# Kernel tuning notes

Measured on AMD Instinct MI355X. Metric: run time of the kernel, lower is better.

Reference implementation:

```python
import jax, jax.numpy as jnp
import numpy as np

N_NODES = 50000
N_EDGES = 800000
IN_CH = 128
HIDDEN = 64
OUT_CH = 32
N_REL = 8
N_GRAPHS = 64
NEG_SLOPE = 0.2  # RGATConv default leaky_relu slope


def setup_inputs() -> dict:
    key = jax.random.key(0)
    ks = jax.random.split(key, 20)
    s = 0.05
    inp = {
        "x": jax.random.normal(ks[0], (N_NODES, IN_CH), dtype=jnp.float32),
        "edge_index": jax.random.randint(ks[1], (2, N_EDGES), 0, N_NODES, dtype=jnp.int64),
        "edge_type": jax.random.randint(ks[2], (N_EDGES,), 0, N_REL, dtype=jnp.int64),
        "batch": jnp.sort(jax.random.randint(ks[3], (N_NODES,), 0, N_GRAPHS, dtype=jnp.int64)),
        # encoder Linear(in, hidden)
        "enc_W": jax.random.normal(ks[4], (IN_CH, HIDDEN), dtype=jnp.float32) * s,
        "enc_b": jnp.zeros((HIDDEN,), dtype=jnp.float32),
        # RGAT layer 0 (hidden -> hidden), heads=1, dim=1
        "w0": jax.random.normal(ks[5], (N_REL, HIDDEN, HIDDEN), dtype=jnp.float32) * s,
        "q0": jax.random.normal(ks[6], (HIDDEN, 1), dtype=jnp.float32) * s,
        "k0": jax.random.normal(ks[7], (HIDDEN, 1), dtype=jnp.float32) * s,
        "b0": jnp.zeros((HIDDEN,), dtype=jnp.float32),
        # RGAT layer 1 (hidden -> hidden)
        "w1": jax.random.normal(ks[8], (N_REL, HIDDEN, HIDDEN), dtype=jnp.float32) * s,
        "q1": jax.random.normal(ks[9], (HIDDEN, 1), dtype=jnp.float32) * s,
        "k1": jax.random.normal(ks[10], (HIDDEN, 1), dtype=jnp.float32) * s,
        "b1": jnp.zeros((HIDDEN,), dtype=jnp.float32),
        # head: Linear(hidden, hidden) + ReLU, then clf Linear(hidden, out)
        "lin_W": jax.random.normal(ks[11], (HIDDEN, HIDDEN), dtype=jnp.float32) * s,
        "lin_b": jnp.zeros((HIDDEN,), dtype=jnp.float32),
        "clf_W": jax.random.normal(ks[12], (HIDDEN, OUT_CH), dtype=jnp.float32) * s,
        "clf_b": jnp.zeros((OUT_CH,), dtype=jnp.float32),
    }
    return inp


def rgat_layer(h, src, dst, etype, w, q, k, b):
    # per-relation transform of all nodes: [R, N, out]
    h_all = jnp.einsum('ni,rio->rno', h, w)
    hi = h_all[etype, dst]          # [E, out] transformed target feats
    hj = h_all[etype, src]          # [E, out] transformed source feats
    # additive self-attention (heads=1, dim=1), across-relation softmax
    alpha = jax.nn.leaky_relu((hi @ q + hj @ k)[:, 0], NEG_SLOPE)  # [E]
    m = jax.ops.segment_max(alpha, dst, num_segments=N_NODES)
    e = jnp.exp(alpha - m[dst])
    ssum = jax.ops.segment_sum(e, dst, num_segments=N_NODES)
    a = e / jnp.maximum(ssum[dst], 1e-16)
    out = jax.ops.segment_sum(a[:, None] * hj, dst, num_segments=N_NODES)
    return out + b


def reference(x, edge_index, edge_type, batch,
              enc_W, enc_b, w0, q0, k0, b0, w1, q1, k1, b1,
              lin_W, lin_b, clf_W, clf_b):
    src, dst = edge_index[0], edge_index[1]
    h = x @ enc_W + enc_b                      # encoder
    h = rgat_layer(h, src, dst, edge_type, w0, q0, k0, b0)
    h = jax.nn.relu(h)                         # inter-layer relu (dropout=0)
    h = rgat_layer(h, src, dst, edge_type, w1, q1, k1, b1)
    pooled = jax.ops.segment_sum(h, batch, num_segments=N_GRAPHS)  # global_add_pool
    z = jax.nn.relu(pooled @ lin_W + lin_b)
    return z @ clf_W + clf_b                   # [N_GRAPHS, OUT_CH]
```

## Files before the change

### kernel.cpp

```cpp
#include <hip/hip_runtime.h>
#include <hip/hip_bf16.h>

#define NN 50000
#define NE 800000
#define INC 128
#define HID 64
#define OUTC 32
#define NREL 8
#define NG 64
#define SLOPE 0.2f
#define NB2 196
#define SCAP 6144

typedef unsigned int uint32;
typedef unsigned short ushort16;
typedef __attribute__((ext_vector_type(8))) short short8;
typedef __attribute__((ext_vector_type(4))) short short4v;
typedef __attribute__((ext_vector_type(4))) float float4v;
typedef __attribute__((ext_vector_type(4))) int int4v;

__device__ __forceinline__ float bf2f(ushort16 u) {
    union { uint32 i; float f; } v; v.i = ((uint32)u) << 16; return v.f;
}
__device__ __forceinline__ ushort16 f2bf(float f) {
    union { float f; uint32 i; } v; v.f = f;
    uint32 i = v.i;
    return (ushort16)((i + 0x7FFFu + ((i >> 16) & 1u)) >> 16);
}

__global__ __launch_bounds__(256) void enc_mfma(const float* __restrict__ x,
    const float* __restrict__ W, const float* __restrict__ bias,
    ushort16* __restrict__ hb)
{
    int tid = threadIdx.x, wv = tid >> 6, lane = tid & 63;
    int g = lane >> 4, lr = lane & 15;

    short8 bf[4][4];
    for (int t = 0; t < 4; ++t)
        for (int kc = 0; kc < 4; ++kc) {
            short8 v;
            #pragma unroll
            for (int j = 0; j < 8; ++j) {
                int k = kc * 32 + g * 8 + j;
                v[j] = (short)f2bf(W[k * HID + t * 16 + lr]);
            }
            bf[t][kc] = v;
        }

    __shared__ float lds[4][16 * 65];
    float* myl = lds[wv];

    for (int tile = blockIdx.x * 4 + wv; tile < NN / 16; tile += gridDim.x * 4) {
        int row0 = tile * 16;
        const float4v* xp = (const float4v*)(x + (size_t)(row0 + lr) * INC);
        short8 af[4];
        #pragma unroll
        for (int kc = 0; kc < 4; ++kc) {
            float4v u0 = xp[kc * 8 + g * 2];
            float4v u1 = xp[kc * 8 + g * 2 + 1];
            short8 v;
            v[0] = (short)f2bf(u0[0]); v[1] = (short)f2bf(u0[1]);
            v[2] = (short)f2bf(u0[2]); v[3] = (short)f2bf(u0[3]);
            v[4] = (short)f2bf(u1[0]); v[5] = (short)f2bf(u1[1]);
            v[6] = (short)f2bf(u1[2]); v[7] = (short)f2bf(u1[3]);
            af[kc] = v;
        }
        float4v acc[4];
        #pragma unroll
        for (int t = 0; t < 4; ++t) { float4v z = {0.f,0.f,0.f,0.f}; acc[t] = z; }
        #pragma unroll
        for (int t = 0; t < 4; ++t)
            #pragma unroll
            for (int kc = 0; kc < 4; ++kc)
                acc[t] = __builtin_amdgcn_mfma_f32_16x16x32_bf16(af[kc], bf[t][kc], acc[t], 0, 0, 0);

        #pragma unroll
        for (int t = 0; t < 4; ++t)
            #pragma unroll
            for (int i = 0; i < 4; ++i)
                myl[(4 * g + i) * 65 + t * 16 + lr] = acc[t][i];
        __asm volatile("s_waitcnt lgkmcnt(0)" ::: "memory");

        int row = lane >> 2, cg = lane & 3;
        const float* srcp = myl + row * 65 + cg * 16;
        uint32 p[8];
        #pragma unroll
        for (int j = 0; j < 8; ++j) {
            float v0 = srcp[2 * j]     + bias[cg * 16 + 2 * j];
            float v1 = srcp[2 * j + 1] + bias[cg * 16 + 2 * j + 1];
            p[j] = (uint32)f2bf(v0) | ((uint32)f2bf(v1) << 16);
        }
        int4v s0 = {(int)p[0], (int)p[1], (int)p[2], (int)p[3]};
        int4v s1 = {(int)p[4], (int)p[5], (int)p[6], (int)p[7]};
        int4v* op = (int4v*)(hb + (size_t)(row0 + row) * HID + cg * 16);
        op[0] = s0; op[1] = s1;
        __asm volatile("s_waitcnt lgkmcnt(0)" ::: "memory");
    }
}

__global__ __launch_bounds__(256) void hall_mfma(const ushort16* __restrict__ hb,
    const float* __restrict__ w, ushort16* __restrict__ hall)
{
    int r = blockIdx.y;
    int tid = threadIdx.x, wv = tid >> 6, lane = tid & 63;
    int g = lane >> 4, lr = lane & 15;
    const float* wr = w + (size_t)r * HID * HID;

    short8 bf[4][2];
    for (int t = 0; t < 4; ++t)
        for (int kc = 0; kc < 2; ++kc) {
            short8 v;
            #pragma unroll
            for (int j = 0; j < 8; ++j) {
                int k = kc * 32 + g * 8 + j;
                v[j] = (short)f2bf(wr[k * HID + t * 16 + lr]);
            }
            bf[t][kc] = v;
        }

    __shared__ float lds[4][16 * 65];
    float* myl = lds[wv];
    ushort16* outr = hall + (size_t)r * NN * HID;

    for (int tile = blockIdx.x * 4 + wv; tile < NN / 16; tile += gridDim.x * 4) {
        int row0 = tile * 16;
        const short8* ap = (const short8*)(hb + (size_t)(row0 + lr) * HID);
        short8 a0 = ap[g];
        short8 a1 = ap[4 + g];
        float4v acc[4];
        #pragma unroll
        for (int t = 0; t < 4; ++t) { float4v z = {0.f,0.f,0.f,0.f}; acc[t] = z; }
        #pragma unroll
        for (int t = 0; t < 4; ++t) {
            acc[t] = __builtin_amdgcn_mfma_f32_16x16x32_bf16(a0, bf[t][0], acc[t], 0, 0, 0);
            acc[t] = __builtin_amdgcn_mfma_f32_16x16x32_bf16(a1, bf[t][1], acc[t], 0, 0, 0);
        }
        #pragma unroll
        for (int t = 0; t < 4; ++t)
            #pragma unroll
            for (int i = 0; i < 4; ++i)
                myl[(4 * g + i) * 65 + t * 16 + lr] = acc[t][i];
        __asm volatile("s_waitcnt lgkmcnt(0)" ::: "memory");

        int row = lane >> 2, cg = lane & 3;
        const float* srcp = myl + row * 65 + cg * 16;
        uint32 p[8];
        #pragma unroll
        for (int j = 0; j < 8; ++j)
            p[j] = (uint32)f2bf(srcp[2 * j]) | ((uint32)f2bf(srcp[2 * j + 1]) << 16);
        int4v s0 = {(int)p[0], (int)p[1], (int)p[2], (int)p[3]};
        int4v s1 = {(int)p[4], (int)p[5], (int)p[6], (int)p[7]};
        int4v* op = (int4v*)(outr + (size_t)(row0 + row) * HID + cg * 16);
        op[0] = s0; op[1] = s1;
        __asm volatile("s_waitcnt lgkmcnt(0)" ::: "memory");
    }
}

__global__ void wqk_kernel(const float* __restrict__ w, const float* __restrict__ q,
                           const float* __restrict__ k, float* __restrict__ wqk)
{
    int j = blockIdx.x;
    int i = threadIdx.x;
    int r = j & 7;
    const float* v = (j < 8) ? q : k;
    const float* wr = w + ((size_t)r * HID + i) * HID;
    float acc = 0.f;
    for (int o = 0; o < HID; ++o) acc += wr[o] * v[o];
    wqk[j * HID + i] = acc;
}

__global__ __launch_bounds__(256) void s_kernel(const ushort16* __restrict__ hb,
    const float* __restrict__ wqk, float* __restrict__ sbuf)
{
    __shared__ float Ws[16 * 65];
    __shared__ short4v Hs[16][17];
    int tid = threadIdx.x;
    for (int i = tid; i < 16 * HID; i += 256) Ws[(i >> 6) * 65 + (i & 63)] = wqk[i];
    int n0 = blockIdx.x * 16;
    {
        int row = tid >> 4, ch = tid & 15;
        Hs[row][ch] = *(const short4v*)(hb + (size_t)(n0 + row) * HID + ch * 4);
    }
    __syncthreads();
    int j = tid & 15, nl = tid >> 4;
    short4v hreg[16];
    #pragma unroll
    for (int c = 0; c < 16; ++c) hreg[c] = Hs[nl][c];
    float acc = 0.f;
    #pragma unroll
    for (int c = 0; c < 16; ++c)
        #pragma unroll
        for (int u = 0; u < 4; ++u)
            acc += bf2f((ushort16)hreg[c][u]) * Ws[j * 65 + c * 4 + u];
    sbuf[(size_t)j * NN + n0 + nl] = acc;
}


__global__ __launch_bounds__(256) void histo196(const int* __restrict__ dst,
                                                int* __restrict__ bucketHist)
{
    __shared__ int lh[NB2];
    int t = threadIdx.x;
    for (int i = t; i < NB2; i += 256) lh[i] = 0;
    __syncthreads();
    int base = blockIdx.x * 2048;
    for (int i = t; i < 2048; i += 256) {
        int idx = base + i;
        if (idx < NE) atomicAdd(&lh[dst[idx] >> 8], 1);
    }
    __syncthreads();
    for (int i = t; i < NB2; i += 256) if (lh[i]) atomicAdd(&bucketHist[i], lh[i]);
}

__global__ __launch_bounds__(256) void scan196(const int* __restrict__ bucketHist,
    int* __restrict__ bucketBase, int* __restrict__ bucket_cur)
{
    __shared__ int ps[256];
    int t = threadIdx.x;
    int v = (t < NB2) ? bucketHist[t] : 0;
    ps[t] = v;
    __syncthreads();
    for (int off = 1; off < 256; off <<= 1) {
        int tv = (t >= off) ? ps[t - off] : 0;
        __syncthreads();
        ps[t] += tv;
        __syncthreads();
    }
    int excl = ps[t] - v;
    if (t < NB2) { bucketBase[t] = excl; bucket_cur[t] = excl; }
    if (t == 0) bucketBase[NB2] = NE;
}

__global__ __launch_bounds__(256) void binpass(const int* __restrict__ src,
    const int* __restrict__ dst, const int* __restrict__ et,
    int* __restrict__ bucket_cur, uint32* __restrict__ ebin)
{
    __shared__ int lh[NB2], lbase[NB2], lcur[NB2];
    int t = threadIdx.x;
    for (int i = t; i < NB2; i += 256) { lh[i] = 0; lcur[i] = 0; }
    __syncthreads();
    int base = blockIdx.x * 4096;
    uint32 rec[16]; int bkt[16];
    #pragma unroll
    for (int i = 0; i < 16; ++i) {
        int idx = base + i * 256 + t;
        bkt[i] = -1;
        if (idx < NE) {
            int s = src[idx], d = dst[idx], r = et[idx];
            rec[i] = (uint32)s | ((uint32)r << 16) | ((uint32)(d & 255) << 19);
            bkt[i] = d >> 8;
            atomicAdd(&lh[bkt[i]], 1);
        }
    }
    __syncthreads();
    for (int i = t; i < NB2; i += 256) if (lh[i]) lbase[i] = atomicAdd(&bucket_cur[i], lh[i]);
    __syncthreads();
    #pragma unroll
    for (int i = 0; i < 16; ++i) {
        if (bkt[i] >= 0) {
            int lpos = atomicAdd(&lcur[bkt[i]], 1);
            ebin[lbase[bkt[i]] + lpos] = rec[i];
        }
    }
}

__global__ __launch_bounds__(256) void sortpass(const uint32* __restrict__ ebin,
    const int* __restrict__ bucketBase, int* __restrict__ rowptr,
    uint32* __restrict__ edges_s)
{
    __shared__ uint32 stage[SCAP];
    __shared__ int cnt256[256], ps[256], cur[256];
    int b = blockIdx.x, t = threadIdx.x;
    int seg0 = bucketBase[b], seg1 = bucketBase[b + 1];
    int cnt = seg1 - seg0;
    cnt256[t] = 0;
    __syncthreads();
    for (int i = t; i < cnt; i += 256) {
        uint32 rec = ebin[seg0 + i];
        atomicAdd(&cnt256[(rec >> 19) & 255], 1);
    }
    __syncthreads();
    int v = cnt256[t];
    ps[t] = v;
    __syncthreads();
    for (int off = 1; off < 256; off <<= 1) {
        int tv = (t >= off) ? ps[t - off] : 0;
        __syncthreads();
        ps[t] += tv;
        __syncthreads();
    }
    int excl = ps[t] - v;
    int node = (b << 8) + t;
    if (node < NN) rowptr[node] = seg0 + excl;
    if (b == NB2 - 1 && t == 0) rowptr[NN] = NE;
    cur[t] = excl;
    __syncthreads();
    for (int i = t; i < cnt; i += 256) {
        uint32 rec = ebin[seg0 + i];
        int lpos = atomicAdd(&cur[(rec >> 19) & 255], 1);
        if (lpos < SCAP) stage[lpos] = rec;
        else edges_s[seg0 + lpos] = rec;
    }
    __syncthreads();
    int lim = cnt < SCAP ? cnt : SCAP;
    for (int i = t; i < lim; i += 256) edges_s[seg0 + i] = stage[i];
}

__global__ __launch_bounds__(256) void agg_kernel(const int* __restrict__ rowptr,
    const uint32* __restrict__ edges, const float* __restrict__ sbuf,
    const ushort16* __restrict__ hall, const float* __restrict__ bias,
    ushort16* __restrict__ out_bf, float* __restrict__ out_f32, int do_relu)
{
    int wv = threadIdx.x >> 6, lane = threadIdx.x & 63;
    int d = blockIdx.x * 4 + wv;
    if (d >= NN) return;
    int row0 = rowptr[d];
    int deg = rowptr[d + 1] - row0;
    int g = lane >> 3, cl = lane & 7;

    float myq = (lane < 8) ? sbuf[lane * NN + d] : 0.f;

    float acc[8];
    #pragma unroll
    for (int u = 0; u < 8; ++u) acc[u] = 0.f;
    float ssum = 0.f;

    for (int base = 0; base < deg; base += 16) {
        int j0 = base + g, j1 = j0 + 8;
        bool v0 = j0 < deg, v1 = j1 < deg;
        uint32 pk0 = v0 ? edges[row0 + j0] : 0u;
        uint32 pk1 = v1 ? edges[row0 + j1] : 0u;
        int s0 = (int)(pk0 & 0xFFFFu), r0 = (int)((pk0 >> 16) & 7u);
        int s1 = (int)(pk1 & 0xFFFFu), r1 = (int)((pk1 >> 16) & 7u);
        float sc0 = sbuf[(8 + r0) * NN + s0];
        float sc1 = sbuf[(8 + r1) * NN + s1];
        short8 hv0 = *(const short8*)(hall + ((size_t)r0 * NN + s0) * HID + cl * 8);
        short8 hv1 = *(const short8*)(hall + ((size_t)r1 * NN + s1) * HID + cl * 8);
        float a0 = __shfl(myq, r0) + sc0; a0 = (a0 > 0.f) ? a0 : SLOPE * a0;
        float a1 = __shfl(myq, r1) + sc1; a1 = (a1 > 0.f) ? a1 : SLOPE * a1;
        float ex0 = v0 ? __expf(a0) : 0.f;
        float ex1 = v1 ? __expf(a1) : 0.f;
        ssum += ex0 + ex1;
        #pragma unroll
        for (int u = 0; u < 8; ++u)
            acc[u] += ex0 * bf2f((ushort16)hv0[u]) + ex1 * bf2f((ushort16)hv1[u]);
    }

    #pragma unroll
    for (int o = 8; o < 64; o <<= 1) {
        ssum += __shfl_xor(ssum, o);
        #pragma unroll
        for (int u = 0; u < 8; ++u) acc[u] += __shfl_xor(acc[u], o);
    }

    if (lane < 8) {
        float inv = 1.f / fmaxf(ssum, 1e-16f);
        float o_[8];
        #pragma unroll
        for (int u = 0; u < 8; ++u) o_[u] = acc[u] * inv + bias[lane * 8 + u];
        if (do_relu) {
            uint32 p[4];
            #pragma unroll
            for (int u = 0; u < 4; ++u) {
                float v0 = fmaxf(o_[2 * u], 0.f);
                float v1 = fmaxf(o_[2 * u + 1], 0.f);
                p[u] = (uint32)f2bf(v0) | ((uint32)f2bf(v1) << 16);
            }
            int4v pk4 = {(int)p[0], (int)p[1], (int)p[2], (int)p[3]};
            *(int4v*)(out_bf + (size_t)d * HID + lane * 8) = pk4;
        } else {
            float4v v0 = {o_[0], o_[1], o_[2], o_[3]};
            float4v v1 = {o_[4], o_[5], o_[6], o_[7]};
            float4v* op = (float4v*)(out_f32 + (size_t)d * HID + lane * 8);
            op[0] = v0; op[1] = v1;
        }
    }
}

__global__ void pool_kernel(const float* __restrict__ h, const int* __restrict__ batch,
                            float* __restrict__ pooled)
{
    int t = blockIdx.x * 256 + threadIdx.x;
    int c = t & 63;
    int chunk = t >> 6;
    if (chunk >= NN / 16) return;
    int n0 = chunk * 16;
    float acc = 0.f;
    int cur = batch[n0];
    for (int n = n0; n < n0 + 16; ++n) {
        int b = batch[n];
        if (b != cur) { atomicAdd(&pooled[cur * HID + c], acc); acc = 0.f; cur = b; }
        acc += h[(size_t)n * HID + c];
    }
    atomicAdd(&pooled[cur * HID + c], acc);
}

__global__ __launch_bounds__(256) void head_kernel(const float* __restrict__ pooled,
    const float* __restrict__ linW, const float* __restrict__ linb,
    const float* __restrict__ clfW, const float* __restrict__ clfb,
    float* __restrict__ out)
{
    __shared__ float z[NG * HID];
    __shared__ float p[NG * HID];
    int tid = threadIdx.x;
    for (int i = tid; i < NG * HID; i += 256) p[i] = pooled[i];
    __syncthreads();
    for (int idx = tid; idx < NG * HID; idx += 256) {
        int g = idx >> 6, c = idx & 63;
        float acc = linb[c];
        for (int k = 0; k < HID; ++k) acc += p[g * HID + k] * linW[k * HID + c];
        z[idx] = fmaxf(acc, 0.f);
    }
    __syncthreads();
    for (int idx = tid; idx < NG * OUTC; idx += 256) {
        int g = idx >> 5, c = idx & 31;
        float acc = clfb[c];
        for (int k = 0; k < HID; ++k) acc += z[g * HID + k] * clfW[k * OUTC + c];
        out[idx] = acc;
    }
}

extern "C" void kernel_launch(void* const* d_in, const int* in_sizes, int n_in,
                              void* d_out, int out_size, void* d_ws, size_t ws_size,
                              hipStream_t stream)
{
    const float* x      = (const float*)d_in[0];
    const int*   eidx   = (const int*)d_in[1];
    const int*   etype  = (const int*)d_in[2];
    const int*   batch  = (const int*)d_in[3];
    const float* enc_W  = (const float*)d_in[4];
    const float* enc_b  = (const float*)d_in[5];
    const float* w0     = (const float*)d_in[6];
    const float* q0     = (const float*)d_in[7];
    const float* k0     = (const float*)d_in[8];
    const float* b0     = (const float*)d_in[9];
    const float* w1     = (const float*)d_in[10];
    const float* q1     = (const float*)d_in[11];
    const float* k1     = (const float*)d_in[12];
    const float* b1     = (const float*)d_in[13];
    const float* lin_W  = (const float*)d_in[14];
    const float* lin_b  = (const float*)d_in[15];
    const float* clf_W  = (const float*)d_in[16];
    const float* clf_b  = (const float*)d_in[17];

    const int* srcp = eidx;
    const int* dstp = eidx + NE;

    char* wsb = (char*)d_ws;
    ushort16* h_bf    = (ushort16*)wsb;                 wsb += (size_t)NN * HID * 2;
    ushort16* hall_bf = (ushort16*)wsb;                 wsb += (size_t)NREL * NN * HID * 2;
    float*    h_f     = (float*)wsb;                    wsb += (size_t)NN * HID * 4;
    float*    sbuf    = (float*)wsb;                    wsb += (size_t)16 * NN * 4;
    float*    wqk     = (float*)wsb;                    wsb += 16 * HID * 4;
    float*    pooled  = (float*)wsb;                    wsb += NG * HID * 4;
    int*      rowptr  = (int*)wsb;                      wsb += (size_t)(NN + 64) * 4;
    int*      bucketHist = (int*)wsb;                   wsb += 256 * 4;
    int*      bucketBase = (int*)wsb;                   wsb += 256 * 4;
    int*      bucket_cur = (int*)wsb;                   wsb += 256 * 4;
    uint32*   ebin    = (uint32*)wsb;                   wsb += (size_t)NE * 4;
    uint32*   edges_s = (uint32*)wsb;                   wsb += (size_t)(NE + 64) * 4;

    hipMemsetAsync(bucketHist, 0, NB2 * 4, stream);
    histo196<<<(NE + 2047) / 2048, 256, 0, stream>>>(dstp, bucketHist);
    scan196<<<1, 256, 0, stream>>>(bucketHist, bucketBase, bucket_cur);
    binpass<<<(NE + 4095) / 4096, 256, 0, stream>>>(srcp, dstp, etype, bucket_cur, ebin);
    sortpass<<<NB2, 256, 0, stream>>>(ebin, bucketBase, rowptr, edges_s);

    enc_mfma<<<512, 256, 0, stream>>>(x, enc_W, enc_b, h_bf);

    wqk_kernel<<<16, 64, 0, stream>>>(w0, q0, k0, wqk);
    s_kernel<<<NN / 16, 256, 0, stream>>>(h_bf, wqk, sbuf);
    hall_mfma<<<dim3(256, NREL), 256, 0, stream>>>(h_bf, w0, hall_bf);
    agg_kernel<<<(NN + 3) / 4, 256, 0, stream>>>(rowptr, edges_s, sbuf, hall_bf, b0,
                                                 h_bf, (float*)nullptr, 1);

    wqk_kernel<<<16, 64, 0, stream>>>(w1, q1, k1, wqk);
    s_kernel<<<NN / 16, 256, 0, stream>>>(h_bf, wqk, sbuf);
    hall_mfma<<<dim3(256, NREL), 256, 0, stream>>>(h_bf, w1, hall_bf);
    agg_kernel<<<(NN + 3) / 4, 256, 0, stream>>>(rowptr, edges_s, sbuf, hall_bf, b1,
                                                 (ushort16*)nullptr, h_f, 0);

    hipMemsetAsync(pooled, 0, (size_t)NG * HID * 4, stream);
    pool_kernel<<<(NN / 16 * HID + 255) / 256, 256, 0, stream>>>(h_f, batch, pooled);
    head_kernel<<<1, 256, 0, stream>>>(pooled, lin_W, lin_b, clf_W, clf_b, (float*)d_out);
}
```

Measured before the change: 192.2 us.

## Aggregate raw features per relation then apply relation weights after aggregation

Drops the per-relation transformed feature tensor (8×N×64 bf16) and its MFMA kernel. The aggregation kernel now gathers untransformed source features into per-relation accumulators and then multiplies the resulting [16 nodes × 512] tile by the stacked transposed relation weights with MFMA. This removes a large write and the scattered gathers from the transformed tensor, at the cost of 8x more accumulator registers and FMAs per edge, plus a shared-memory staging step. Weight prep, the attention-vector precompute and the memset work are folded into one prep kernel and into the scan kernel to cut launches.

```diff
diff --git a/kernel.cpp b/kernel.cpp
--- a/kernel.cpp
+++ b/kernel.cpp
@@ -18,6 +18,7 @@
 typedef __attribute__((ext_vector_type(4))) short short4v;
 typedef __attribute__((ext_vector_type(4))) float float4v;
 typedef __attribute__((ext_vector_type(4))) int int4v;
+typedef __attribute__((ext_vector_type(2))) int int2v;
 
 __device__ __forceinline__ float bf2f(ushort16 u) {
     union { uint32 i; float f; } v; v.i = ((uint32)u) << 16; return v.f;
@@ -98,75 +99,39 @@
     }
 }
 
-__global__ __launch_bounds__(256) void hall_mfma(const ushort16* __restrict__ hb,
-    const float* __restrict__ w, ushort16* __restrict__ hall)
-{
-    int r = blockIdx.y;
-    int tid = threadIdx.x, wv = tid >> 6, lane = tid & 63;
-    int g = lane >> 4, lr = lane & 15;
-    const float* wr = w + (size_t)r * HID * HID;
-
-    short8 bf[4][2];
-    for (int t = 0; t < 4; ++t)
-        for (int kc = 0; kc < 2; ++kc) {
-            short8 v;
-            #pragma unroll
-            for (int j = 0; j < 8; ++j) {
-                int k = kc * 32 + g * 8 + j;
-                v[j] = (short)f2bf(wr[k * HID + t * 16 + lr]);
-            }
-            bf[t][kc] = v;
-        }
-
-    __shared__ float lds[4][16 * 65];
-    float* myl = lds[wv];
-    ushort16* outr = hall + (size_t)r * NN * HID;
-
-    for (int tile = blockIdx.x * 4 + wv; tile < NN / 16; tile += gridDim.x * 4) {
-        int row0 = tile * 16;
-        const short8* ap = (const short8*)(hb + (size_t)(row0 + lr) * HID);
-        short8 a0 = ap[g];
-        short8 a1 = ap[4 + g];
-        float4v acc[4];
-        #pragma unroll
-        for (int t = 0; t < 4; ++t) { float4v z = {0.f,0.f,0.f,0.f}; acc[t] = z; }
-        #pragma unroll
-        for (int t = 0; t < 4; ++t) {
-            acc[t] = __builtin_amdgcn_mfma_f32_16x16x32_bf16(a0, bf[t][0], acc[t], 0, 0, 0);
-            acc[t] = __builtin_amdgcn_mfma_f32_16x16x32_bf16(a1, bf[t][1], acc[t], 0, 0, 0);
-        }
-        #pragma unroll
-        for (int t = 0; t < 4; ++t)
-            #pragma unroll
-            for (int i = 0; i < 4; ++i)
-                myl[(4 * g + i) * 65 + t * 16 + lr] = acc[t][i];
-        __asm volatile("s_waitcnt lgkmcnt(0)" ::: "memory");
-
-        int row = lane >> 2, cg = lane & 3;
-        const float* srcp = myl + row * 65 + cg * 16;
-        uint32 p[8];
-        #pragma unroll
-        for (int j = 0; j < 8; ++j)
-            p[j] = (uint32)f2bf(srcp[2 * j]) | ((uint32)f2bf(srcp[2 * j + 1]) << 16);
-        int4v s0 = {(int)p[0], (int)p[1], (int)p[2], (int)p[3]};
-        int4v s1 = {(int)p[4], (int)p[5], (int)p[6], (int)p[7]};
-        int4v* op = (int4v*)(outr + (size_t)(row0 + row) * HID + cg * 16);
-        op[0] = s0; op[1] = s1;
-        __asm volatile("s_waitcnt lgkmcnt(0)" ::: "memory");
-    }
-}
-
-__global__ void wqk_kernel(const float* __restrict__ w, const float* __restrict__ q,
-                           const float* __restrict__ k, float* __restrict__ wqk)
-{
-    int j = blockIdx.x;
-    int i = threadIdx.x;
-    int r = j & 7;
-    const float* v = (j < 8) ? q : k;
-    const float* wr = w + ((size_t)r * HID + i) * HID;
-    float acc = 0.f;
-    for (int o = 0; o < HID; ++o) acc += wr[o] * v[o];
-    wqk[j * HID + i] = acc;
+__global__ __launch_bounds__(256) void prep_kernel(
+    const float* __restrict__ w0, const float* __restrict__ q0, const float* __restrict__ k0,
+    const float* __restrict__ w1, const float* __restrict__ q1, const float* __restrict__ k1,
+    float* __restrict__ wqk0, float* __restrict__ wqk1,
+    ushort16* __restrict__ wbfT0, ushort16* __restrict__ wbfT1,
+    int* __restrict__ bucketHist)
+{
+    int b = blockIdx.x, t = threadIdx.x;
+    if (b < 32) {
+        const float* w  = (b < 16) ? w0 : w1;
+        const float* qv = (b < 16) ? q0 : q1;
+        const float* kv = (b < 16) ? k0 : k1;
+        float* out = (b < 16) ? wqk0 : wqk1;
+        int j = b & 15;
+        int r = j & 7;
+        const float* vv = (j < 8) ? qv : kv;
+        if (t < 64) {
+            const float* wr = w + ((size_t)r * HID + t) * HID;
+            float acc = 0.f;
+            for (int o = 0; o < HID; ++o) acc += wr[o] * vv[o];
+            out[j * HID + t] = acc;
+        }
+    } else if (b < 96) {
+        int o = b - 32;
+        for (int k2 = t; k2 < 512; k2 += 256)
+            wbfT0[(size_t)o * 512 + k2] = f2bf(w0[(size_t)k2 * HID + o]);
+    } else if (b < 160) {
+        int o = b - 96;
+        for (int k2 = t; k2 < 512; k2 += 256)
+            wbfT1[(size_t)o * 512 + k2] = f2bf(w1[(size_t)k2 * HID + o]);
+    } else {
+        if (t < NB2) bucketHist[t] = 0;
+    }
 }
 
 __global__ __launch_bounds__(256) void s_kernel(const ushort16* __restrict__ hb,
@@ -195,7 +160,6 @@
     sbuf[(size_t)j * NN + n0 + nl] = acc;
 }
 
-
 __global__ __launch_bounds__(256) void histo196(const int* __restrict__ dst,
                                                 int* __restrict__ bucketHist)
 {
@@ -213,7 +177,8 @@
 }
 
 __global__ __launch_bounds__(256) void scan196(const int* __restrict__ bucketHist,
-    int* __restrict__ bucketBase, int* __restrict__ bucket_cur)
+    int* __restrict__ bucketBase, int* __restrict__ bucket_cur,
+    float* __restrict__ pooled)
 {
     __shared__ int ps[256];
     int t = threadIdx.x;
@@ -229,6 +194,8 @@
     int excl = ps[t] - v;
     if (t < NB2) { bucketBase[t] = excl; bucket_cur[t] = excl; }
     if (t == 0) bucketBase[NB2] = NE;
+    #pragma unroll
+    for (int i = 0; i < (NG * HID) / 256; ++i) pooled[i * 256 + t] = 0.f;
 }
 
 __global__ __launch_bounds__(256) void binpass(const int* __restrict__ src,
@@ -306,73 +273,109 @@
     for (int i = t; i < lim; i += 256) edges_s[seg0 + i] = stage[i];
 }
 
-__global__ __launch_bounds__(256) void agg_kernel(const int* __restrict__ rowptr,
+template<int LAYER>
+__global__ __launch_bounds__(256) void agg3_kernel(const int* __restrict__ rowptr,
     const uint32* __restrict__ edges, const float* __restrict__ sbuf,
-    const ushort16* __restrict__ hall, const float* __restrict__ bias,
-    ushort16* __restrict__ out_bf, float* __restrict__ out_f32, int do_relu)
-{
-    int wv = threadIdx.x >> 6, lane = threadIdx.x & 63;
-    int d = blockIdx.x * 4 + wv;
-    if (d >= NN) return;
-    int row0 = rowptr[d];
-    int deg = rowptr[d + 1] - row0;
-    int g = lane >> 3, cl = lane & 7;
-
-    float myq = (lane < 8) ? sbuf[lane * NN + d] : 0.f;
-
-    float acc[8];
-    #pragma unroll
-    for (int u = 0; u < 8; ++u) acc[u] = 0.f;
-    float ssum = 0.f;
-
-    for (int base = 0; base < deg; base += 16) {
-        int j0 = base + g, j1 = j0 + 8;
-        bool v0 = j0 < deg, v1 = j1 < deg;
-        uint32 pk0 = v0 ? edges[row0 + j0] : 0u;
-        uint32 pk1 = v1 ? edges[row0 + j1] : 0u;
-        int s0 = (int)(pk0 & 0xFFFFu), r0 = (int)((pk0 >> 16) & 7u);
-        int s1 = (int)(pk1 & 0xFFFFu), r1 = (int)((pk1 >> 16) & 7u);
-        float sc0 = sbuf[(8 + r0) * NN + s0];
-        float sc1 = sbuf[(8 + r1) * NN + s1];
-        short8 hv0 = *(const short8*)(hall + ((size_t)r0 * NN + s0) * HID + cl * 8);
-        short8 hv1 = *(const short8*)(hall + ((size_t)r1 * NN + s1) * HID + cl * 8);
-        float a0 = __shfl(myq, r0) + sc0; a0 = (a0 > 0.f) ? a0 : SLOPE * a0;
-        float a1 = __shfl(myq, r1) + sc1; a1 = (a1 > 0.f) ? a1 : SLOPE * a1;
-        float ex0 = v0 ? __expf(a0) : 0.f;
-        float ex1 = v1 ? __expf(a1) : 0.f;
-        ssum += ex0 + ex1;
-        #pragma unroll
-        for (int u = 0; u < 8; ++u)
-            acc[u] += ex0 * bf2f((ushort16)hv0[u]) + ex1 * bf2f((ushort16)hv1[u]);
-    }
-
-    #pragma unroll
-    for (int o = 8; o < 64; o <<= 1) {
-        ssum += __shfl_xor(ssum, o);
-        #pragma unroll
-        for (int u = 0; u < 8; ++u) acc[u] += __shfl_xor(acc[u], o);
-    }
-
-    if (lane < 8) {
+    const ushort16* __restrict__ hsrc, const ushort16* __restrict__ wbfT,
+    const float* __restrict__ bias, ushort16* __restrict__ out_bf,
+    float* __restrict__ out_f)
+{
+    int tid = threadIdx.x, wv = tid >> 6, lane = tid & 63;
+    int g = lane >> 4, cl = lane & 15;
+    __shared__ ushort16 A[32][520];
+
+    short8 Bf[16];
+    int bcol = wv * 16 + cl;
+    #pragma unroll
+    for (int kc = 0; kc < 16; ++kc)
+        Bf[kc] = *(const short8*)(wbfT + (size_t)bcol * 512 + kc * 32 + g * 8);
+
+    int d0 = blockIdx.x * 16 + wv * 4;
+    #pragma unroll 1
+    for (int rr = 0; rr < 4; ++rr) {
+        int d = d0 + rr;
+        int row0 = rowptr[d];
+        int deg  = rowptr[d + 1] - row0;
+        float myq = (lane < 8) ? sbuf[lane * NN + d] : 0.f;
+
+        float accR[8][4];
+        #pragma unroll
+        for (int r8 = 0; r8 < 8; ++r8)
+            #pragma unroll
+            for (int u = 0; u < 4; ++u) accR[r8][u] = 0.f;
+        float ssum = 0.f;
+
+        for (int base = 0; base < deg; base += 8) {
+            int j0 = base + g, j1 = base + 4 + g;
+            bool v0 = j0 < deg, v1 = j1 < deg;
+            uint32 pk0 = v0 ? edges[row0 + j0] : 0u;
+            uint32 pk1 = v1 ? edges[row0 + j1] : 0u;
+            int s0 = (int)(pk0 & 0xFFFFu), r0 = (int)((pk0 >> 16) & 7u);
+            int s1 = (int)(pk1 & 0xFFFFu), r1 = (int)((pk1 >> 16) & 7u);
+            float sc0 = sbuf[(8 + r0) * NN + s0];
+            float sc1 = sbuf[(8 + r1) * NN + s1];
+            short4v hv0 = *(const short4v*)(hsrc + (size_t)s0 * HID + cl * 4);
+            short4v hv1 = *(const short4v*)(hsrc + (size_t)s1 * HID + cl * 4);
+            float a0 = __shfl(myq, r0) + sc0; a0 = (a0 > 0.f) ? a0 : SLOPE * a0;
+            float a1 = __shfl(myq, r1) + sc1; a1 = (a1 > 0.f) ? a1 : SLOPE * a1;
+            float ex0 = v0 ? __expf(a0) : 0.f;
+            float ex1 = v1 ? __expf(a1) : 0.f;
+            ssum += ex0 + ex1;
+            float h00 = bf2f((ushort16)hv0[0]), h01 = bf2f((ushort16)hv0[1]);
+            float h02 = bf2f((ushort16)hv0[2]), h03 = bf2f((ushort16)hv0[3]);
+            float h10 = bf2f((ushort16)hv1[0]), h11 = bf2f((ushort16)hv1[1]);
+            float h12 = bf2f((ushort16)hv1[2]), h13 = bf2f((ushort16)hv1[3]);
+            #pragma unroll
+            for (int r8 = 0; r8 < 8; ++r8) {
+                float e0 = (r0 == r8) ? ex0 : 0.f;
+                float e1 = (r1 == r8) ? ex1 : 0.f;
+                accR[r8][0] += e0 * h00 + e1 * h10;
+                accR[r8][1] += e0 * h01 + e1 * h11;
+                accR[r8][2] += e0 * h02 + e1 * h12;
+                accR[r8][3] += e0 * h03 + e1 * h13;
+            }
+        }
+
+        ssum += __shfl_xor(ssum, 16);
+        ssum += __shfl_xor(ssum, 32);
+        #pragma unroll
+        for (int r8 = 0; r8 < 8; ++r8)
+            #pragma unroll
+            for (int u = 0; u < 4; ++u)
+                accR[r8][u] += __shfl_xor(accR[r8][u], 16);
         float inv = 1.f / fmaxf(ssum, 1e-16f);
-        float o_[8];
-        #pragma unroll
-        for (int u = 0; u < 8; ++u) o_[u] = acc[u] * inv + bias[lane * 8 + u];
-        if (do_relu) {
-            uint32 p[4];
-            #pragma unroll
-            for (int u = 0; u < 4; ++u) {
-                float v0 = fmaxf(o_[2 * u], 0.f);
-                float v1 = fmaxf(o_[2 * u + 1], 0.f);
-                p[u] = (uint32)f2bf(v0) | ((uint32)f2bf(v1) << 16);
+
+        if ((g & 1) == 0) {
+            int arow = (wv * 4 + rr) + ((g >> 1) << 4);
+            ushort16* ap = &A[arow][0];
+            #pragma unroll
+            for (int r8 = 0; r8 < 8; ++r8) {
+                uint32 lo = (uint32)f2bf(accR[r8][0] * inv) | ((uint32)f2bf(accR[r8][1] * inv) << 16);
+                uint32 hi = (uint32)f2bf(accR[r8][2] * inv) | ((uint32)f2bf(accR[r8][3] * inv) << 16);
+                int2v pk2 = {(int)lo, (int)hi};
+                *(int2v*)(ap + r8 * HID + cl * 4) = pk2;
             }
-            int4v pk4 = {(int)p[0], (int)p[1], (int)p[2], (int)p[3]};
-            *(int4v*)(out_bf + (size_t)d * HID + lane * 8) = pk4;
+        }
+    }
+    __syncthreads();
+
+    float4v c4 = {0.f, 0.f, 0.f, 0.f};
+    #pragma unroll
+    for (int kc = 0; kc < 16; ++kc) {
+        short8 a1 = *(const short8*)(&A[cl][kc * 32 + g * 8]);
+        c4 = __builtin_amdgcn_mfma_f32_16x16x32_bf16(a1, Bf[kc], c4, 0, 0, 0);
+        short8 a2 = *(const short8*)(&A[16 + cl][kc * 32 + g * 8]);
+        c4 = __builtin_amdgcn_mfma_f32_16x16x32_bf16(a2, Bf[kc], c4, 0, 0, 0);
+    }
+    float bb = bias[bcol];
+    #pragma unroll
+    for (int i = 0; i < 4; ++i) {
+        int drow = blockIdx.x * 16 + 4 * g + i;
+        float val = c4[i] + bb;
+        if (LAYER == 0) {
+            out_bf[(size_t)drow * HID + bcol] = f2bf(fmaxf(val, 0.f));
         } else {
-            float4v v0 = {o_[0], o_[1], o_[2], o_[3]};
-            float4v v1 = {o_[4], o_[5], o_[6], o_[7]};
-            float4v* op = (float4v*)(out_f32 + (size_t)d * HID + lane * 8);
-            op[0] = v0; op[1] = v1;
+            out_f[(size_t)drow * HID + bcol] = val;
         }
     }
 }
@@ -448,10 +451,13 @@
 
     char* wsb = (char*)d_ws;
     ushort16* h_bf    = (ushort16*)wsb;                 wsb += (size_t)NN * HID * 2;
-    ushort16* hall_bf = (ushort16*)wsb;                 wsb += (size_t)NREL * NN * HID * 2;
+    ushort16* h2_bf   = (ushort16*)wsb;                 wsb += (size_t)NN * HID * 2;
     float*    h_f     = (float*)wsb;                    wsb += (size_t)NN * HID * 4;
     float*    sbuf    = (float*)wsb;                    wsb += (size_t)16 * NN * 4;
-    float*    wqk     = (float*)wsb;                    wsb += 16 * HID * 4;
+    float*    wqk0    = (float*)wsb;                    wsb += 16 * HID * 4;
+    float*    wqk1    = (float*)wsb;                    wsb += 16 * HID * 4;
+    ushort16* wbfT0   = (ushort16*)wsb;                 wsb += (size_t)HID * 512 * 2;
+    ushort16* wbfT1   = (ushort16*)wsb;                 wsb += (size_t)HID * 512 * 2;
     float*    pooled  = (float*)wsb;                    wsb += NG * HID * 4;
     int*      rowptr  = (int*)wsb;                      wsb += (size_t)(NN + 64) * 4;
     int*      bucketHist = (int*)wsb;                   wsb += 256 * 4;
@@ -460,27 +466,24 @@
     uint32*   ebin    = (uint32*)wsb;                   wsb += (size_t)NE * 4;
     uint32*   edges_s = (uint32*)wsb;                   wsb += (size_t)(NE + 64) * 4;
 
-    hipMemsetAsync(bucketHist, 0, NB2 * 4, stream);
+    prep_kernel<<<161, 256, 0, stream>>>(w0, q0, k0, w1, q1, k1,
+                                         wqk0, wqk1, wbfT0, wbfT1, bucketHist);
+
     histo196<<<(NE + 2047) / 2048, 256, 0, stream>>>(dstp, bucketHist);
-    scan196<<<1, 256, 0, stream>>>(bucketHist, bucketBase, bucket_cur);
+    scan196<<<1, 256, 0, stream>>>(bucketHist, bucketBase, bucket_cur, pooled);
     binpass<<<(NE + 4095) / 4096, 256, 0, stream>>>(srcp, dstp, etype, bucket_cur, ebin);
     sortpass<<<NB2, 256, 0, stream>>>(ebin, bucketBase, rowptr, edges_s);
 
     enc_mfma<<<512, 256, 0, stream>>>(x, enc_W, enc_b, h_bf);
 
-    wqk_kernel<<<16, 64, 0, stream>>>(w0, q0, k0, wqk);
-    s_kernel<<<NN / 16, 256, 0, stream>>>(h_bf, wqk, sbuf);
-    hall_mfma<<<dim3(256, NREL), 256, 0, stream>>>(h_bf, w0, hall_bf);
-    agg_kernel<<<(NN + 3) / 4, 256, 0, stream>>>(rowptr, edges_s, sbuf, hall_bf, b0,
-                                                 h_bf, (float*)nullptr, 1);
-
-    wqk_kernel<<<16, 64, 0, stream>>>(w1, q1, k1, wqk);
-    s_kernel<<<NN / 16, 256, 0, stream>>>(h_bf, wqk, sbuf);
-    hall_mfma<<<dim3(256, NREL), 256, 0, stream>>>(h_bf, w1, hall_bf);
-    agg_kernel<<<(NN + 3) / 4, 256, 0, stream>>>(rowptr, edges_s, sbuf, hall_bf, b1,
-                                                 (ushort16*)nullptr, h_f, 0);
-
-    hipMemsetAsync(pooled, 0, (size_t)NG * HID * 4, stream);
+    s_kernel<<<NN / 16, 256, 0, stream>>>(h_bf, wqk0, sbuf);
+    agg3_kernel<0><<<NN / 16, 256, 0, stream>>>(rowptr, edges_s, sbuf, h_bf, wbfT0,
+                                                b0, h2_bf, (float*)nullptr);
+
+    s_kernel<<<NN / 16, 256, 0, stream>>>(h2_bf, wqk1, sbuf);
+    agg3_kernel<1><<<NN / 16, 256, 0, stream>>>(rowptr, edges_s, sbuf, h2_bf, wbfT1,
+                                                b1, (ushort16*)nullptr, h_f);
+
     pool_kernel<<<(NN / 16 * HID + 255) / 256, 256, 0, stream>>>(h_f, batch, pooled);
     head_kernel<<<1, 256, 0, stream>>>(pooled, lin_W, lin_b, clf_W, clf_b, (float*)d_out);
 }
```

New measurement: 276.0 us. +43.6%, slower.

## Merge launches: fused prep, combined score/transform kernel, per-graph pooled head

Applied to the files above, without the earlier changes.

Both layers' wqk projections and the histogram zeroing now run in one prep kernel, replacing two small kernels and a memset. The per-node score kernel and the per-relation MFMA transform share one grid, with block index choosing the role. Pooling and the MLP head become a single kernel with one block per graph, which finds its node range by binary search on the sorted batch vector and avoids atomics. The aim is to cut launch count and the tail bubbles between dependent small kernels. The cost is more shared memory per block in the merged kernel, which may lower occupancy, and a pooling pass limited to 64 blocks.

```diff
diff --git a/kernel.cpp b/kernel.cpp
--- a/kernel.cpp
+++ b/kernel.cpp
@@ -11,6 +11,7 @@
 #define SLOPE 0.2f
 #define NB2 196
 #define SCAP 6144
+#define S_BLOCKS (NN / 16)
 
 typedef unsigned int uint32;
 typedef unsigned short ushort16;
@@ -98,15 +99,44 @@
     }
 }
 
-__global__ __launch_bounds__(256) void hall_mfma(const ushort16* __restrict__ hb,
-    const float* __restrict__ w, ushort16* __restrict__ hall)
-{
-    int r = blockIdx.y;
-    int tid = threadIdx.x, wv = tid >> 6, lane = tid & 63;
+__global__ __launch_bounds__(256) void sh_kernel(const ushort16* __restrict__ hb,
+    const float* __restrict__ wqk, const float* __restrict__ w,
+    float* __restrict__ sbuf, ushort16* __restrict__ hall)
+{
+    __shared__ float lds4[4][16 * 65];
+    __shared__ float Ws[16 * 65];
+    __shared__ short4v Hs[16][17];
+    int tid = threadIdx.x;
+
+    if (blockIdx.x < S_BLOCKS) {
+        for (int i = tid; i < 16 * HID; i += 256) Ws[(i >> 6) * 65 + (i & 63)] = wqk[i];
+        int n0 = blockIdx.x * 16;
+        {
+            int row = tid >> 4, ch = tid & 15;
+            Hs[row][ch] = *(const short4v*)(hb + (size_t)(n0 + row) * HID + ch * 4);
+        }
+        __syncthreads();
+        int j = tid & 15, nl = tid >> 4;
+        short4v hreg[16];
+        #pragma unroll
+        for (int c = 0; c < 16; ++c) hreg[c] = Hs[nl][c];
+        float acc = 0.f;
+        #pragma unroll
+        for (int c = 0; c < 16; ++c)
+            #pragma unroll
+            for (int u = 0; u < 4; ++u)
+                acc += bf2f((ushort16)hreg[c][u]) * Ws[j * 65 + c * 4 + u];
+        sbuf[(size_t)j * NN + n0 + nl] = acc;
+        return;
+    }
+
+    int b = blockIdx.x - S_BLOCKS;
+    int r = b >> 9, xb = b & 511;
+    int wv = tid >> 6, lane = tid & 63;
     int g = lane >> 4, lr = lane & 15;
     const float* wr = w + (size_t)r * HID * HID;
 
-    short8 bf[4][2];
+    short8 bfr[4][2];
     for (int t = 0; t < 4; ++t)
         for (int kc = 0; kc < 2; ++kc) {
             short8 v;
@@ -115,14 +145,13 @@
                 int k = kc * 32 + g * 8 + j;
                 v[j] = (short)f2bf(wr[k * HID + t * 16 + lr]);
             }
-            bf[t][kc] = v;
-        }
-
-    __shared__ float lds[4][16 * 65];
-    float* myl = lds[wv];
+            bfr[t][kc] = v;
+        }
+
+    float* myl = lds4[wv];
     ushort16* outr = hall + (size_t)r * NN * HID;
 
-    for (int tile = blockIdx.x * 4 + wv; tile < NN / 16; tile += gridDim.x * 4) {
+    for (int tile = xb * 4 + wv; tile < NN / 16; tile += 512 * 4) {
         int row0 = tile * 16;
         const short8* ap = (const short8*)(hb + (size_t)(row0 + lr) * HID);
         short8 a0 = ap[g];
@@ -132,8 +161,8 @@
         for (int t = 0; t < 4; ++t) { float4v z = {0.f,0.f,0.f,0.f}; acc[t] = z; }
         #pragma unroll
         for (int t = 0; t < 4; ++t) {
-            acc[t] = __builtin_amdgcn_mfma_f32_16x16x32_bf16(a0, bf[t][0], acc[t], 0, 0, 0);
-            acc[t] = __builtin_amdgcn_mfma_f32_16x16x32_bf16(a1, bf[t][1], acc[t], 0, 0, 0);
+            acc[t] = __builtin_amdgcn_mfma_f32_16x16x32_bf16(a0, bfr[t][0], acc[t], 0, 0, 0);
+            acc[t] = __builtin_amdgcn_mfma_f32_16x16x32_bf16(a1, bfr[t][1], acc[t], 0, 0, 0);
         }
         #pragma unroll
         for (int t = 0; t < 4; ++t)
@@ -156,45 +185,31 @@
     }
 }
 
-__global__ void wqk_kernel(const float* __restrict__ w, const float* __restrict__ q,
-                           const float* __restrict__ k, float* __restrict__ wqk)
-{
-    int j = blockIdx.x;
-    int i = threadIdx.x;
-    int r = j & 7;
-    const float* v = (j < 8) ? q : k;
-    const float* wr = w + ((size_t)r * HID + i) * HID;
-    float acc = 0.f;
-    for (int o = 0; o < HID; ++o) acc += wr[o] * v[o];
-    wqk[j * HID + i] = acc;
-}
-
-__global__ __launch_bounds__(256) void s_kernel(const ushort16* __restrict__ hb,
-    const float* __restrict__ wqk, float* __restrict__ sbuf)
-{
-    __shared__ float Ws[16 * 65];
-    __shared__ short4v Hs[16][17];
-    int tid = threadIdx.x;
-    for (int i = tid; i < 16 * HID; i += 256) Ws[(i >> 6) * 65 + (i & 63)] = wqk[i];
-    int n0 = blockIdx.x * 16;
-    {
-        int row = tid >> 4, ch = tid & 15;
-        Hs[row][ch] = *(const short4v*)(hb + (size_t)(n0 + row) * HID + ch * 4);
-    }
-    __syncthreads();
-    int j = tid & 15, nl = tid >> 4;
-    short4v hreg[16];
-    #pragma unroll
-    for (int c = 0; c < 16; ++c) hreg[c] = Hs[nl][c];
-    float acc = 0.f;
-    #pragma unroll
-    for (int c = 0; c < 16; ++c)
-        #pragma unroll
-        for (int u = 0; u < 4; ++u)
-            acc += bf2f((ushort16)hreg[c][u]) * Ws[j * 65 + c * 4 + u];
-    sbuf[(size_t)j * NN + n0 + nl] = acc;
-}
-
+__global__ __launch_bounds__(256) void prep_kernel(
+    const float* __restrict__ w0, const float* __restrict__ q0, const float* __restrict__ k0,
+    const float* __restrict__ w1, const float* __restrict__ q1, const float* __restrict__ k1,
+    float* __restrict__ wqk0, float* __restrict__ wqk1,
+    int* __restrict__ bucketHist)
+{
+    int b = blockIdx.x, t = threadIdx.x;
+    if (b < 32) {
+        const float* w  = (b < 16) ? w0 : w1;
+        const float* qv = (b < 16) ? q0 : q1;
+        const float* kv = (b < 16) ? k0 : k1;
+        float* out = (b < 16) ? wqk0 : wqk1;
+        int j = b & 15;
+        int r = j & 7;
+        const float* vv = (j < 8) ? qv : kv;
+        if (t < 64) {
+            const float* wr = w + ((size_t)r * HID + t) * HID;
+            float acc = 0.f;
+            for (int o = 0; o < HID; ++o) acc += wr[o] * vv[o];
+            out[j * HID + t] = acc;
+        }
+    } else {
+        if (t < NB2) bucketHist[t] = 0;
+    }
+}
 
 __global__ __launch_bounds__(256) void histo196(const int* __restrict__ dst,
                                                 int* __restrict__ bucketHist)
@@ -377,46 +392,42 @@
     }
 }
 
-__global__ void pool_kernel(const float* __restrict__ h, const int* __restrict__ batch,
-                            float* __restrict__ pooled)
-{
-    int t = blockIdx.x * 256 + threadIdx.x;
-    int c = t & 63;
-    int chunk = t >> 6;
-    if (chunk >= NN / 16) return;
-    int n0 = chunk * 16;
-    float acc = 0.f;
-    int cur = batch[n0];
-    for (int n = n0; n < n0 + 16; ++n) {
-        int b = batch[n];
-        if (b != cur) { atomicAdd(&pooled[cur * HID + c], acc); acc = 0.f; cur = b; }
-        acc += h[(size_t)n * HID + c];
-    }
-    atomicAdd(&pooled[cur * HID + c], acc);
-}
-
-__global__ __launch_bounds__(256) void head_kernel(const float* __restrict__ pooled,
+__global__ __launch_bounds__(256) void head2_kernel(const float* __restrict__ h,
+    const int* __restrict__ batch,
     const float* __restrict__ linW, const float* __restrict__ linb,
     const float* __restrict__ clfW, const float* __restrict__ clfb,
     float* __restrict__ out)
 {
-    __shared__ float z[NG * HID];
-    __shared__ float p[NG * HID];
-    int tid = threadIdx.x;
-    for (int i = tid; i < NG * HID; i += 256) p[i] = pooled[i];
-    __syncthreads();
-    for (int idx = tid; idx < NG * HID; idx += 256) {
-        int g = idx >> 6, c = idx & 63;
-        float acc = linb[c];
-        for (int k = 0; k < HID; ++k) acc += p[g * HID + k] * linW[k * HID + c];
-        z[idx] = fmaxf(acc, 0.f);
-    }
-    __syncthreads();
-    for (int idx = tid; idx < NG * OUTC; idx += 256) {
-        int g = idx >> 5, c = idx & 31;
-        float acc = clfb[c];
-        for (int k = 0; k < HID; ++k) acc += z[g * HID + k] * clfW[k * OUTC + c];
-        out[idx] = acc;
+    int gidx = blockIdx.x, t = threadIdx.x;
+    int a = 0, b = NN;
+    while (a < b) { int m = (a + b) >> 1; if (batch[m] < gidx) a = m + 1; else b = m; }
+    int lo = a;
+    b = NN;
+    while (a < b) { int m = (a + b) >> 1; if (batch[m] < gidx + 1) a = m + 1; else b = m; }
+    int hi = a;
+
+    int c = t & 63, rg = t >> 6;
+    float acc = 0.f;
+    for (int n = lo + rg; n < hi; n += 4) acc += h[(size_t)n * HID + c];
+    __shared__ float part[4][64];
+    __shared__ float pooled[64];
+    __shared__ float z[64];
+    part[rg][c] = acc;
+    __syncthreads();
+    if (t < 64) pooled[t] = (part[0][t] + part[1][t]) + (part[2][t] + part[3][t]);
+    __syncthreads();
+    if (t < 64) {
+        float a2 = linb[t];
+        #pragma unroll 8
+        for (int k = 0; k < HID; ++k) a2 += pooled[k] * linW[k * HID + t];
+        z[t] = fmaxf(a2, 0.f);
+    }
+    __syncthreads();
+    if (t < 32) {
+        float a3 = clfb[t];
+        #pragma unroll 8
+        for (int k = 0; k < HID; ++k) a3 += z[k] * clfW[k * OUTC + t];
+        out[gidx * OUTC + t] = a3;
     }
 }
 
@@ -451,8 +462,8 @@
     ushort16* hall_bf = (ushort16*)wsb;                 wsb += (size_t)NREL * NN * HID * 2;
     float*    h_f     = (float*)wsb;                    wsb += (size_t)NN * HID * 4;
     float*    sbuf    = (float*)wsb;                    wsb += (size_t)16 * NN * 4;
-    float*    wqk     = (float*)wsb;                    wsb += 16 * HID * 4;
-    float*    pooled  = (float*)wsb;                    wsb += NG * HID * 4;
+    float*    wqk0    = (float*)wsb;                    wsb += 16 * HID * 4;
+    float*    wqk1    = (float*)wsb;                    wsb += 16 * HID * 4;
     int*      rowptr  = (int*)wsb;                      wsb += (size_t)(NN + 64) * 4;
     int*      bucketHist = (int*)wsb;                   wsb += 256 * 4;
     int*      bucketBase = (int*)wsb;                   wsb += 256 * 4;
@@ -460,7 +471,8 @@
     uint32*   ebin    = (uint32*)wsb;                   wsb += (size_t)NE * 4;
     uint32*   edges_s = (uint32*)wsb;                   wsb += (size_t)(NE + 64) * 4;
 
-    hipMemsetAsync(bucketHist, 0, NB2 * 4, stream);
+    prep_kernel<<<33, 256, 0, stream>>>(w0, q0, k0, w1, q1, k1, wqk0, wqk1, bucketHist);
+
     histo196<<<(NE + 2047) / 2048, 256, 0, stream>>>(dstp, bucketHist);
     scan196<<<1, 256, 0, stream>>>(bucketHist, bucketBase, bucket_cur);
     binpass<<<(NE + 4095) / 4096, 256, 0, stream>>>(srcp, dstp, etype, bucket_cur, ebin);
@@ -468,19 +480,16 @@
 
     enc_mfma<<<512, 256, 0, stream>>>(x, enc_W, enc_b, h_bf);
 
-    wqk_kernel<<<16, 64, 0, stream>>>(w0, q0, k0, wqk);
-    s_kernel<<<NN / 16, 256, 0, stream>>>(h_bf, wqk, sbuf);
-    hall_mfma<<<dim3(256, NREL), 256, 0, stream>>>(h_bf, w0, hall_bf);
+    const int SH_GRID = S_BLOCKS + 512 * NREL;
+
+    sh_kernel<<<SH_GRID, 256, 0, stream>>>(h_bf, wqk0, w0, sbuf, hall_bf);
     agg_kernel<<<(NN + 3) / 4, 256, 0, stream>>>(rowptr, edges_s, sbuf, hall_bf, b0,
                                                  h_bf, (float*)nullptr, 1);
 
-    wqk_kernel<<<16, 64, 0, stream>>>(w1, q1, k1, wqk);
-    s_kernel<<<NN / 16, 256, 0, stream>>>(h_bf, wqk, sbuf);
-    hall_mfma<<<dim3(256, NREL), 256, 0, stream>>>(h_bf, w1, hall_bf);
+    sh_kernel<<<SH_GRID, 256, 0, stream>>>(h_bf, wqk1, w1, sbuf, hall_bf);
     agg_kernel<<<(NN + 3) / 4, 256, 0, stream>>>(rowptr, edges_s, sbuf, hall_bf, b1,
                                                  (ushort16*)nullptr, h_f, 0);
 
-    hipMemsetAsync(pooled, 0, (size_t)NG * HID * 4, stream);
-    pool_kernel<<<(NN / 16 * HID + 255) / 256, 256, 0, stream>>>(h_f, batch, pooled);
-    head_kernel<<<1, 256, 0, stream>>>(pooled, lin_W, lin_b, clf_W, clf_b, (float*)d_out);
-}
+    head2_kernel<<<NG, 256, 0, stream>>>(h_f, batch, lin_W, lin_b, clf_W, clf_b,
+                                         (float*)d_out);
+}
```

Result: slower. 221.4 us (+15.2%).
